# Kernel optimization log

Measured on AMD Instinct MI355X. Metric: run time of the kernel, lower is better.

Reference implementation:

```python
import jax, jax.numpy as jnp
import numpy as np

MOMENTUM = 0.9
EPS = 1e-12


def l2norm(x, axis=-1):
    # matches torch F.normalize: x / max(||x||, eps)
    n = jnp.sqrt(jnp.sum(x * x, axis=axis, keepdims=True))
    return x / jnp.maximum(n, EPS)


def setup_inputs() -> dict:
    key = jax.random.key(0)
    k1, k2, k3 = jax.random.split(key, 3)
    N, C, D = 65536, 1024, 512
    feats = jax.random.normal(k1, (N, D), dtype=jnp.float32)
    prototypes = l2norm(jax.random.normal(k2, (C, D), dtype=jnp.float32))
    labels = jax.random.randint(k3, (N,), 0, C, dtype=jnp.int64)
    return {"feats": feats, "prototypes": prototypes, "labels": labels}


def reference(feats, prototypes, labels):
    C = prototypes.shape[0]
    f = l2norm(feats)  # [N, D]
    # segment-mean per class (vectorized replacement of the Python loop)
    sums = jax.ops.segment_sum(f, labels, num_segments=C)          # [C, D]
    counts = jax.ops.segment_sum(jnp.ones((f.shape[0],), f.dtype), labels,
                                 num_segments=C)                    # [C]
    mean_c = sums / jnp.maximum(counts, 1.0)[:, None]               # [C, D]
    # EMA update + renormalize, only where class present in batch
    ema = l2norm(MOMENTUM * prototypes + (1.0 - MOMENTUM) * mean_c)
    new_protos = jnp.where((counts > 0)[:, None], ema, prototypes)  # [C, D]
    # similarity against updated bank
    sim = jnp.einsum('nd,cd->nc', f, new_protos)                    # [N, C]
    return sim
```

## Files before the change

### kernel.cpp

```cpp
#include <hip/hip_runtime.h>
#include <cstdint>
#include <cstddef>

typedef short short8 __attribute__((ext_vector_type(8)));
typedef float floatx4 __attribute__((ext_vector_type(4)));
typedef unsigned short ushort4v __attribute__((ext_vector_type(4)));
typedef unsigned short ushort2v __attribute__((ext_vector_type(2)));

#define AS1C(p) ((const __attribute__((address_space(1))) void*)(p))
#define AS3(p)  ((__attribute__((address_space(3))) void*)(p))

__device__ __forceinline__ unsigned short f2bf(float f) {
    union { float f; unsigned int u; } v; v.f = f;
    unsigned int u = v.u;
    unsigned int r = (u + 0x7fffu + ((u >> 16) & 1u)) >> 16;
    return (unsigned short)r;
}

__device__ __forceinline__ float bf2f(unsigned short b) {
    union { unsigned int u; float f; } v;
    v.u = (unsigned int)b << 16;
    return v.f;
}

__device__ __forceinline__ float wave_sum(float s) {
#pragma unroll
    for (int off = 32; off > 0; off >>= 1)
        s += __shfl_xor(s, off, 64);
    return s;
}

__global__ __launch_bounds__(256) void k_norm(
    const float* __restrict__ feats, const int* __restrict__ labels,
    unsigned short* __restrict__ fb, int* __restrict__ cnt,
    int* __restrict__ idx2, int N)
{
    const int gw   = (int)((blockIdx.x * 256u + threadIdx.x) >> 6);
    const int lane = threadIdx.x & 63;
    if (gw >= N) return;

    const float* row = feats + (size_t)gw * 512;
    floatx4 x0 = *(const floatx4*)(row + lane * 4);
    floatx4 x1 = *(const floatx4*)(row + 256 + lane * 4);

    float s = x0.x * x0.x + x0.y * x0.y + x0.z * x0.z + x0.w * x0.w
            + x1.x * x1.x + x1.y * x1.y + x1.z * x1.z + x1.w * x1.w;
    s = wave_sum(s);
    const float inv = 1.0f / fmaxf(sqrtf(s), 1e-12f);

    floatx4 y0 = x0 * inv, y1 = x1 * inv;

    ushort4v b0, b1;
    b0.x = f2bf(y0.x); b0.y = f2bf(y0.y); b0.z = f2bf(y0.z); b0.w = f2bf(y0.w);
    b1.x = f2bf(y1.x); b1.y = f2bf(y1.y); b1.z = f2bf(y1.z); b1.w = f2bf(y1.w);
    *(ushort4v*)(fb + (size_t)gw * 512 + lane * 4)       = b0;
    *(ushort4v*)(fb + (size_t)gw * 512 + 256 + lane * 4) = b1;

    if (lane == 0) {
        const int lab = labels[gw];
        const int pos = atomicAdd(cnt + lab, 1);
        if (pos < 512) idx2[lab * 512 + pos] = gw;
    }
}

__global__ __launch_bounds__(256) void k_segsum_update(
    const unsigned short* __restrict__ fb, const int* __restrict__ idx2,
    const int* __restrict__ cnt, const float* __restrict__ protos,
    unsigned short* __restrict__ pb)
{
    const int c = blockIdx.x;
    const int t = threadIdx.x;
    const int n  = cnt[c];
    const int nr = n < 512 ? n : 512;
    const int* lst = idx2 + c * 512;

    float a0 = 0.0f, a1 = 0.0f;
    int j = 0;
    for (; j + 4 <= nr; j += 4) {
        const int4 r = *(const int4*)(lst + j);
        const ushort2v v0 = *(const ushort2v*)(fb + (size_t)r.x * 512 + t * 2);
        const ushort2v v1 = *(const ushort2v*)(fb + (size_t)r.y * 512 + t * 2);
        const ushort2v v2 = *(const ushort2v*)(fb + (size_t)r.z * 512 + t * 2);
        const ushort2v v3 = *(const ushort2v*)(fb + (size_t)r.w * 512 + t * 2);
        a0 += bf2f(v0.x) + bf2f(v1.x) + bf2f(v2.x) + bf2f(v3.x);
        a1 += bf2f(v0.y) + bf2f(v1.y) + bf2f(v2.y) + bf2f(v3.y);
    }
    for (; j < nr; ++j) {
        const int r = lst[j];
        const ushort2v v = *(const ushort2v*)(fb + (size_t)r * 512 + t * 2);
        a0 += bf2f(v.x);
        a1 += bf2f(v.y);
    }

    const float2 p = *(const float2*)(protos + (size_t)c * 512 + t * 2);
    const float rc = 0.1f / fmaxf((float)n, 1.0f);
    const float v0 = 0.9f * p.x + rc * a0;
    const float v1 = 0.9f * p.y + rc * a1;

    __shared__ float red[256];
    red[t] = v0 * v0 + v1 * v1;
    __syncthreads();
#pragma unroll
    for (int off = 128; off > 0; off >>= 1) {
        if (t < off) red[t] += red[t + off];
        __syncthreads();
    }
    const float inv = 1.0f / fmaxf(sqrtf(red[0]), 1e-12f);

    float o0, o1;
    if (n > 0) { o0 = v0 * inv; o1 = v1 * inv; }
    else       { o0 = p.x;      o1 = p.y;      }

    ushort2v b;
    b.x = f2bf(o0);
    b.y = f2bf(o1);
    *(ushort2v*)(pb + (size_t)c * 512 + t * 2) = b;
}

__global__ __launch_bounds__(512, 2) void k_gemm(
    const unsigned short* __restrict__ A, const unsigned short* __restrict__ B,
    float* __restrict__ out, int N, int C)
{
    constexpr int K  = 512;
    constexpr int NT = 8;
    __shared__ unsigned short lds[2][4][128 * 64];

    const int tid  = threadIdx.x;
    const int lane = tid & 63;
    const int wid  = tid >> 6;
    const int wm   = wid >> 2;
    const int wn   = wid & 3;
    const int quad = lane >> 4, l16 = lane & 15;
    const int lofs = l16 * 32 + ((quad * 8) ^ ((l16 >> 3) << 4));
    const int bRow = (wn & 1) * 4;

    const size_t m0 = (size_t)blockIdx.y * 256;
    const size_t n0 = (size_t)blockIdx.x * 256;

    int pre[2], dstG[2];
#pragma unroll
    for (int i = 0; i < 2; ++i) {
        const int G   = i * 512 + tid;
        const int r15 = (G & 63) >> 2;
        const int row = (G >> 7) * 16 + r15;
        const int cbl = (G & 3) ^ (((r15 >> 3) & 1) << 1);
        const int col = ((G >> 6) & 1) * 32 + cbl * 8;
        pre[i]  = row * K + col;
        dstG[i] = G * 8;
    }

#define STAGE(mat, rowbase, k0, slotp) do {                                        \
    _Pragma("unroll")                                                              \
    for (int i_ = 0; i_ < 2; ++i_)                                                 \
        __builtin_amdgcn_global_load_lds(                                          \
            AS1C((mat) + (size_t)(rowbase) * K + (k0) + pre[i_]),                  \
            AS3((slotp) + dstG[i_]), 16, 0, 0);                                    \
} while (0)

    floatx4 acc[8][4];
#pragma unroll
    for (int m = 0; m < 8; ++m)
#pragma unroll
        for (int n = 0; n < 4; ++n)
            acc[m][n] = (floatx4){0.0f, 0.0f, 0.0f, 0.0f};

    STAGE(B, n0,       0,  &lds[0][2][0]);
    STAGE(B, n0 + 128, 0,  &lds[0][3][0]);
    STAGE(A, m0,       0,  &lds[0][0][0]);
    STAGE(A, m0 + 128, 0,  &lds[0][1][0]);
    STAGE(B, n0,       64, &lds[1][2][0]);
    STAGE(B, n0 + 128, 64, &lds[1][3][0]);
    STAGE(A, m0,       64, &lds[1][0][0]);
    asm volatile("s_waitcnt vmcnt(6)" ::: "memory");
    __builtin_amdgcn_s_barrier();

#pragma unroll
    for (int kt = 0; kt < NT; ++kt) {
        const int buf = kt & 1;
        const unsigned short* sA = &lds[buf][wm][0];
        const unsigned short* sB = &lds[buf][2 + (wn >> 1)][0];

        short8 bfr[4][2];
        short8 ac[2][2];
        short8 a3[2][2];

#pragma unroll
        for (int n = 0; n < 4; ++n)
#pragma unroll
            for (int s = 0; s < 2; ++s)
                bfr[n][s] = *(const short8*)(sB + ((bRow + n) << 10) + (s << 9) + lofs);
#pragma unroll
        for (int ml = 0; ml < 2; ++ml)
#pragma unroll
            for (int s = 0; s < 2; ++s)
                ac[ml][s] = *(const short8*)(sA + ((0 + ml) << 10) + (s << 9) + lofs);
        if (kt + 1 < NT) STAGE(A, m0 + 128, (kt + 1) * 64, &lds[buf ^ 1][1][0]);
        __builtin_amdgcn_s_barrier();
        asm volatile("s_waitcnt lgkmcnt(0)" ::: "memory");
        __builtin_amdgcn_sched_barrier(0);
        __builtin_amdgcn_s_setprio(1);
#pragma unroll
        for (int ml = 0; ml < 2; ++ml)
#pragma unroll
            for (int n = 0; n < 4; ++n)
#pragma unroll
                for (int s = 0; s < 2; ++s)
                    acc[0 + ml][n] = __builtin_amdgcn_mfma_f32_16x16x32_bf16(ac[ml][s], bfr[n][s], acc[0 + ml][n], 0, 0, 0);
        __builtin_amdgcn_s_setprio(0);
        __builtin_amdgcn_sched_barrier(0);
        __builtin_amdgcn_s_barrier();

#pragma unroll
        for (int ml = 0; ml < 2; ++ml)
#pragma unroll
            for (int s = 0; s < 2; ++s)
                ac[ml][s] = *(const short8*)(sA + ((2 + ml) << 10) + (s << 9) + lofs);
        if (kt + 2 < NT) STAGE(B, n0, (kt + 2) * 64, &lds[buf][2][0]);
        __builtin_amdgcn_s_barrier();
        asm volatile("s_waitcnt lgkmcnt(0)" ::: "memory");
        __builtin_amdgcn_sched_barrier(0);
        __builtin_amdgcn_s_setprio(1);
#pragma unroll
        for (int ml = 0; ml < 2; ++ml)
#pragma unroll
            for (int n = 0; n < 4; ++n)
#pragma unroll
                for (int s = 0; s < 2; ++s)
                    acc[2 + ml][n] = __builtin_amdgcn_mfma_f32_16x16x32_bf16(ac[ml][s], bfr[n][s], acc[2 + ml][n], 0, 0, 0);
        __builtin_amdgcn_s_setprio(0);
        __builtin_amdgcn_sched_barrier(0);
        __builtin_amdgcn_s_barrier();

#pragma unroll
        for (int ml = 0; ml < 2; ++ml)
#pragma unroll
            for (int s = 0; s < 2; ++s)
                ac[ml][s] = *(const short8*)(sA + ((4 + ml) << 10) + (s << 9) + lofs);
#pragma unroll
        for (int ml = 0; ml < 2; ++ml)
#pragma unroll
            for (int s = 0; s < 2; ++s)
                a3[ml][s] = *(const short8*)(sA + ((6 + ml) << 10) + (s << 9) + lofs);
        if (kt + 2 < NT) STAGE(B, n0 + 128, (kt + 2) * 64, &lds[buf][3][0]);
        __builtin_amdgcn_s_barrier();
        asm volatile("s_waitcnt lgkmcnt(0)" ::: "memory");
        __builtin_amdgcn_sched_barrier(0);
        __builtin_amdgcn_s_setprio(1);
#pragma unroll
        for (int ml = 0; ml < 2; ++ml)
#pragma unroll
            for (int n = 0; n < 4; ++n)
#pragma unroll
                for (int s = 0; s < 2; ++s)
                    acc[4 + ml][n] = __builtin_amdgcn_mfma_f32_16x16x32_bf16(ac[ml][s], bfr[n][s], acc[4 + ml][n], 0, 0, 0);
        __builtin_amdgcn_s_setprio(0);
        __builtin_amdgcn_sched_barrier(0);
        __builtin_amdgcn_s_barrier();

        if (kt + 2 < NT) {
            STAGE(A, m0, (kt + 2) * 64, &lds[buf][0][0]);
            asm volatile("s_waitcnt vmcnt(6)" ::: "memory");
        } else {
            asm volatile("s_waitcnt vmcnt(0)" ::: "memory");
        }
        __builtin_amdgcn_s_barrier();
        asm volatile("s_waitcnt lgkmcnt(0)" ::: "memory");
        __builtin_amdgcn_sched_barrier(0);
        __builtin_amdgcn_s_setprio(1);
#pragma unroll
        for (int ml = 0; ml < 2; ++ml)
#pragma unroll
            for (int n = 0; n < 4; ++n)
#pragma unroll
                for (int s = 0; s < 2; ++s)
                    acc[6 + ml][n] = __builtin_amdgcn_mfma_f32_16x16x32_bf16(a3[ml][s], bfr[n][s], acc[6 + ml][n], 0, 0, 0);
        __builtin_amdgcn_s_setprio(0);
        __builtin_amdgcn_sched_barrier(0);
        __builtin_amdgcn_s_barrier();
    }
#undef STAGE

#pragma unroll
    for (int m = 0; m < 8; ++m) {
        const size_t r0 = m0 + (size_t)(wm * 128 + m * 16 + quad * 4);
#pragma unroll
        for (int n = 0; n < 4; ++n) {
            const size_t c = n0 + (size_t)(wn * 64 + n * 16 + l16);
#pragma unroll
            for (int r = 0; r < 4; ++r)
                out[(r0 + r) * (size_t)C + c] = acc[m][n][r];
        }
    }
}

extern "C" void kernel_launch(void* const* d_in, const int* in_sizes, int n_in,
                              void* d_out, int out_size, void* d_ws, size_t ws_size,
                              hipStream_t stream)
{
    const float* feats  = (const float*)d_in[0];
    const float* protos = (const float*)d_in[1];
    const int*   labels = (const int*)d_in[2];
    float* sim = (float*)d_out;

    const int D = 512;
    const int N = in_sizes[0] / D;
    const int C = in_sizes[1] / D;

    char* w = (char*)d_ws;
    unsigned short* fb = (unsigned short*)w;
    size_t off = (size_t)N * D * 2;
    unsigned short* pb = (unsigned short*)(w + off);
    off += (size_t)C * D * 2;
    int* idx2 = (int*)(w + off);
    off += (size_t)C * 512 * 4;
    int* cnt = (int*)(w + off);

    hipMemsetAsync(cnt, 0, (size_t)C * 4, stream);

    k_norm<<<dim3(N / 4), dim3(256), 0, stream>>>(feats, labels, fb, cnt, idx2, N);
    k_segsum_update<<<dim3(C), dim3(256), 0, stream>>>(fb, idx2, cnt, protos, pb);

    dim3 g(C / 256, N / 256);
    k_gemm<<<g, dim3(512), 0, stream>>>(fb, pb, sim, N, C);
}
```

Baseline: 433.2 us.

## Halve GEMM K-tile to 32 to cut LDS and raise occupancy target

Shrinks the K-step of the bf16 MFMA GEMM from 64 to 32, which halves the LDS footprint per block. Launch bounds are raised from 2 to 4 blocks per CU to fit more waves. The LDS XOR swizzle is removed, and the fully unrolled k-loop becomes a non-unrolled loop over pairs of macro-expanded tiles. The intent is more occupancy and smaller code, at the cost of twice as many barriers per K, possible LDS bank conflicts without the swizzle, and register pressure under the tighter launch bound that may cause spills.

```diff
diff --git a/kernel.cpp b/kernel.cpp
--- a/kernel.cpp
+++ b/kernel.cpp
@@ -117,13 +117,13 @@
     *(ushort2v*)(pb + (size_t)c * 512 + t * 2) = b;
 }
 
-__global__ __launch_bounds__(512, 2) void k_gemm(
+__global__ __launch_bounds__(512, 4) void k_gemm(
     const unsigned short* __restrict__ A, const unsigned short* __restrict__ B,
     float* __restrict__ out, int N, int C)
 {
     constexpr int K  = 512;
-    constexpr int NT = 8;
-    __shared__ unsigned short lds[2][4][128 * 64];
+    constexpr int NT = 16;
+    __shared__ unsigned short lds[2][4][128 * 32];
 
     const int tid  = threadIdx.x;
     const int lane = tid & 63;
@@ -131,31 +131,19 @@
     const int wm   = wid >> 2;
     const int wn   = wid & 3;
     const int quad = lane >> 4, l16 = lane & 15;
-    const int lofs = l16 * 32 + ((quad * 8) ^ ((l16 >> 3) << 4));
+    const int lofs = l16 * 32 + quad * 8;
     const int bRow = (wn & 1) * 4;
 
     const size_t m0 = (size_t)blockIdx.y * 256;
     const size_t n0 = (size_t)blockIdx.x * 256;
 
-    int pre[2], dstG[2];
-#pragma unroll
-    for (int i = 0; i < 2; ++i) {
-        const int G   = i * 512 + tid;
-        const int r15 = (G & 63) >> 2;
-        const int row = (G >> 7) * 16 + r15;
-        const int cbl = (G & 3) ^ (((r15 >> 3) & 1) << 1);
-        const int col = ((G >> 6) & 1) * 32 + cbl * 8;
-        pre[i]  = row * K + col;
-        dstG[i] = G * 8;
-    }
-
-#define STAGE(mat, rowbase, k0, slotp) do {                                        \
-    _Pragma("unroll")                                                              \
-    for (int i_ = 0; i_ < 2; ++i_)                                                 \
-        __builtin_amdgcn_global_load_lds(                                          \
-            AS1C((mat) + (size_t)(rowbase) * K + (k0) + pre[i_]),                  \
-            AS3((slotp) + dstG[i_]), 16, 0, 0);                                    \
-} while (0)
+    const int preOfs = (tid >> 2) * K + (tid & 3) * 8;
+    const int dstOfs = tid * 8;
+
+#define STAGE(mat, rowbase, k0, slotp)                                          \
+    __builtin_amdgcn_global_load_lds(                                           \
+        AS1C((mat) + (size_t)(rowbase) * K + (k0) + preOfs),                    \
+        AS3((slotp) + dstOfs), 16, 0, 0)
 
     floatx4 acc[8][4];
 #pragma unroll
@@ -163,121 +151,101 @@
 #pragma unroll
         for (int n = 0; n < 4; ++n)
             acc[m][n] = (floatx4){0.0f, 0.0f, 0.0f, 0.0f};
+
+#define MFMA8(R0, AR)                                                           \
+    _Pragma("unroll")                                                           \
+    for (int m_ = 0; m_ < 2; ++m_)                                              \
+        _Pragma("unroll")                                                       \
+        for (int n_ = 0; n_ < 4; ++n_)                                          \
+            acc[(R0) + m_][n_] = __builtin_amdgcn_mfma_f32_16x16x32_bf16(       \
+                AR[m_], bfr[n_], acc[(R0) + m_][n_], 0, 0, 0)
+
+#define GTILE(KT, BUF, P0STAGE, KT2STAGE) do {                                  \
+    const unsigned short* sA = &lds[BUF][wm][0];                                \
+    const unsigned short* sB = &lds[BUF][2 + (wn >> 1)][0];                     \
+    short8 bfr[4], ac[2], a3[2];                                                \
+               \
+    _Pragma("unroll")                                                           \
+    for (int n_ = 0; n_ < 4; ++n_)                                              \
+        bfr[n_] = *(const short8*)(sB + ((bRow + n_) << 9) + lofs);             \
+    _Pragma("unroll")                                                           \
+    for (int m_ = 0; m_ < 2; ++m_)                                              \
+        ac[m_] = *(const short8*)(sA + (m_ << 9) + lofs);                       \
+    if (P0STAGE) STAGE(A, m0 + 128, ((KT) + 1) * 32, &lds[(BUF) ^ 1][1][0]);    \
+    __builtin_amdgcn_s_barrier();                                               \
+    asm volatile("s_waitcnt lgkmcnt(0)" ::: "memory");                          \
+    __builtin_amdgcn_sched_barrier(0);                                          \
+    __builtin_amdgcn_s_setprio(1);                                              \
+    MFMA8(0, ac);                                                               \
+    __builtin_amdgcn_s_setprio(0);                                              \
+    __builtin_amdgcn_sched_barrier(0);                                          \
+    __builtin_amdgcn_s_barrier();                                               \
+                        \
+    _Pragma("unroll")                                                           \
+    for (int m_ = 0; m_ < 2; ++m_)                                              \
+        ac[m_] = *(const short8*)(sA + ((2 + m_) << 9) + lofs);                 \
+    if (KT2STAGE) STAGE(B, n0, ((KT) + 2) * 32, &lds[BUF][2][0]);               \
+    __builtin_amdgcn_s_barrier();                                               \
+    asm volatile("s_waitcnt lgkmcnt(0)" ::: "memory");                          \
+    __builtin_amdgcn_sched_barrier(0);                                          \
+    __builtin_amdgcn_s_setprio(1);                                              \
+    MFMA8(2, ac);                                                               \
+    __builtin_amdgcn_s_setprio(0);                                              \
+    __builtin_amdgcn_sched_barrier(0);                                          \
+    __builtin_amdgcn_s_barrier();                                               \
+        \
+    _Pragma("unroll")                                                           \
+    for (int m_ = 0; m_ < 2; ++m_)                                              \
+        ac[m_] = *(const short8*)(sA + ((4 + m_) << 9) + lofs);                 \
+    _Pragma("unroll")                                                           \
+    for (int m_ = 0; m_ < 2; ++m_)                                              \
+        a3[m_] = *(const short8*)(sA + ((6 + m_) << 9) + lofs);                 \
+    if (KT2STAGE) STAGE(B, n0 + 128, ((KT) + 2) * 32, &lds[BUF][3][0]);         \
+    __builtin_amdgcn_s_barrier();                                               \
+    asm volatile("s_waitcnt lgkmcnt(0)" ::: "memory");                          \
+    __builtin_amdgcn_sched_barrier(0);                                          \
+    __builtin_amdgcn_s_setprio(1);                                              \
+    MFMA8(4, ac);                                                               \
+    __builtin_amdgcn_s_setprio(0);                                              \
+    __builtin_amdgcn_sched_barrier(0);                                          \
+    __builtin_amdgcn_s_barrier();                                               \
+         \
+    if (KT2STAGE) {                                                             \
+        STAGE(A, m0, ((KT) + 2) * 32, &lds[BUF][0][0]);                         \
+        asm volatile("s_waitcnt vmcnt(3)" ::: "memory");                        \
+    } else {                                                                    \
+        asm volatile("s_waitcnt vmcnt(0)" ::: "memory");                        \
+    }                                                                           \
+    __builtin_amdgcn_s_barrier();                                               \
+    asm volatile("s_waitcnt lgkmcnt(0)" ::: "memory");                          \
+    __builtin_amdgcn_sched_barrier(0);                                          \
+    __builtin_amdgcn_s_setprio(1);                                              \
+    MFMA8(6, a3);                                                               \
+    __builtin_amdgcn_s_setprio(0);                                              \
+    __builtin_amdgcn_sched_barrier(0);                                          \
+    __builtin_amdgcn_s_barrier();                                               \
+} while (0)
 
     STAGE(B, n0,       0,  &lds[0][2][0]);
     STAGE(B, n0 + 128, 0,  &lds[0][3][0]);
     STAGE(A, m0,       0,  &lds[0][0][0]);
     STAGE(A, m0 + 128, 0,  &lds[0][1][0]);
-    STAGE(B, n0,       64, &lds[1][2][0]);
-    STAGE(B, n0 + 128, 64, &lds[1][3][0]);
-    STAGE(A, m0,       64, &lds[1][0][0]);
-    asm volatile("s_waitcnt vmcnt(6)" ::: "memory");
+    STAGE(B, n0,       32, &lds[1][2][0]);
+    STAGE(B, n0 + 128, 32, &lds[1][3][0]);
+    STAGE(A, m0,       32, &lds[1][0][0]);
+    asm volatile("s_waitcnt vmcnt(3)" ::: "memory");
     __builtin_amdgcn_s_barrier();
 
-#pragma unroll
-    for (int kt = 0; kt < NT; ++kt) {
-        const int buf = kt & 1;
-        const unsigned short* sA = &lds[buf][wm][0];
-        const unsigned short* sB = &lds[buf][2 + (wn >> 1)][0];
-
-        short8 bfr[4][2];
-        short8 ac[2][2];
-        short8 a3[2][2];
-
-#pragma unroll
-        for (int n = 0; n < 4; ++n)
-#pragma unroll
-            for (int s = 0; s < 2; ++s)
-                bfr[n][s] = *(const short8*)(sB + ((bRow + n) << 10) + (s << 9) + lofs);
-#pragma unroll
-        for (int ml = 0; ml < 2; ++ml)
-#pragma unroll
-            for (int s = 0; s < 2; ++s)
-                ac[ml][s] = *(const short8*)(sA + ((0 + ml) << 10) + (s << 9) + lofs);
-        if (kt + 1 < NT) STAGE(A, m0 + 128, (kt + 1) * 64, &lds[buf ^ 1][1][0]);
-        __builtin_amdgcn_s_barrier();
-        asm volatile("s_waitcnt lgkmcnt(0)" ::: "memory");
-        __builtin_amdgcn_sched_barrier(0);
-        __builtin_amdgcn_s_setprio(1);
-#pragma unroll
-        for (int ml = 0; ml < 2; ++ml)
-#pragma unroll
-            for (int n = 0; n < 4; ++n)
-#pragma unroll
-                for (int s = 0; s < 2; ++s)
-                    acc[0 + ml][n] = __builtin_amdgcn_mfma_f32_16x16x32_bf16(ac[ml][s], bfr[n][s], acc[0 + ml][n], 0, 0, 0);
-        __builtin_amdgcn_s_setprio(0);
-        __builtin_amdgcn_sched_barrier(0);
-        __builtin_amdgcn_s_barrier();
-
-#pragma unroll
-        for (int ml = 0; ml < 2; ++ml)
-#pragma unroll
-            for (int s = 0; s < 2; ++s)
-                ac[ml][s] = *(const short8*)(sA + ((2 + ml) << 10) + (s << 9) + lofs);
-        if (kt + 2 < NT) STAGE(B, n0, (kt + 2) * 64, &lds[buf][2][0]);
-        __builtin_amdgcn_s_barrier();
-        asm volatile("s_waitcnt lgkmcnt(0)" ::: "memory");
-        __builtin_amdgcn_sched_barrier(0);
-        __builtin_amdgcn_s_setprio(1);
-#pragma unroll
-        for (int ml = 0; ml < 2; ++ml)
-#pragma unroll
-            for (int n = 0; n < 4; ++n)
-#pragma unroll
-                for (int s = 0; s < 2; ++s)
-                    acc[2 + ml][n] = __builtin_amdgcn_mfma_f32_16x16x32_bf16(ac[ml][s], bfr[n][s], acc[2 + ml][n], 0, 0, 0);
-        __builtin_amdgcn_s_setprio(0);
-        __builtin_amdgcn_sched_barrier(0);
-        __builtin_amdgcn_s_barrier();
-
-#pragma unroll
-        for (int ml = 0; ml < 2; ++ml)
-#pragma unroll
-            for (int s = 0; s < 2; ++s)
-                ac[ml][s] = *(const short8*)(sA + ((4 + ml) << 10) + (s << 9) + lofs);
-#pragma unroll
-        for (int ml = 0; ml < 2; ++ml)
-#pragma unroll
-            for (int s = 0; s < 2; ++s)
-                a3[ml][s] = *(const short8*)(sA + ((6 + ml) << 10) + (s << 9) + lofs);
-        if (kt + 2 < NT) STAGE(B, n0 + 128, (kt + 2) * 64, &lds[buf][3][0]);
-        __builtin_amdgcn_s_barrier();
-        asm volatile("s_waitcnt lgkmcnt(0)" ::: "memory");
-        __builtin_amdgcn_sched_barrier(0);
-        __builtin_amdgcn_s_setprio(1);
-#pragma unroll
-        for (int ml = 0; ml < 2; ++ml)
-#pragma unroll
-            for (int n = 0; n < 4; ++n)
-#pragma unroll
-                for (int s = 0; s < 2; ++s)
-                    acc[4 + ml][n] = __builtin_amdgcn_mfma_f32_16x16x32_bf16(ac[ml][s], bfr[n][s], acc[4 + ml][n], 0, 0, 0);
-        __builtin_amdgcn_s_setprio(0);
-        __builtin_amdgcn_sched_barrier(0);
-        __builtin_amdgcn_s_barrier();
-
-        if (kt + 2 < NT) {
-            STAGE(A, m0, (kt + 2) * 64, &lds[buf][0][0]);
-            asm volatile("s_waitcnt vmcnt(6)" ::: "memory");
-        } else {
-            asm volatile("s_waitcnt vmcnt(0)" ::: "memory");
-        }
-        __builtin_amdgcn_s_barrier();
-        asm volatile("s_waitcnt lgkmcnt(0)" ::: "memory");
-        __builtin_amdgcn_sched_barrier(0);
-        __builtin_amdgcn_s_setprio(1);
-#pragma unroll
-        for (int ml = 0; ml < 2; ++ml)
-#pragma unroll
-            for (int n = 0; n < 4; ++n)
-#pragma unroll
-                for (int s = 0; s < 2; ++s)
-                    acc[6 + ml][n] = __builtin_amdgcn_mfma_f32_16x16x32_bf16(a3[ml][s], bfr[n][s], acc[6 + ml][n], 0, 0, 0);
-        __builtin_amdgcn_s_setprio(0);
-        __builtin_amdgcn_sched_barrier(0);
-        __builtin_amdgcn_s_barrier();
-    }
+#pragma unroll 1
+    for (int kt = 0; kt < NT - 2; kt += 2) {
+        GTILE(kt,     0, 1, 1);
+        GTILE(kt + 1, 1, 1, 1);
+    }
+    GTILE(NT - 2, 0, 1, 0);
+    GTILE(NT - 1, 1, 0, 0);
+
+#undef GTILE
+#undef MFMA8
 #undef STAGE
 
 #pragma unroll
```

After: 1.024 ms. +136.3%, slower.
